# Optimization experiments

Measured on AMD Instinct MI355X. Metric: run time of the kernel, lower is better.

The kernel has to match this reference:

```python
import jax, jax.numpy as jnp
import numpy as np

B, S, E, H = 4, 2048, 1024, 16
D = E // H  # head_dim = 64

def setup_inputs() -> dict:
    key = jax.random.key(0)
    k1, k2, k3 = jax.random.split(key, 3)
    x = jax.random.normal(k1, (B, S, E), dtype=jnp.float32)
    # Linear weights stored as [in, out] so y = x @ W (torch Linear uses W^T; same math).
    w_att = jax.random.normal(k2, (E, 3 * E), dtype=jnp.float32) * (1.0 / np.sqrt(E))
    w_proj = jax.random.normal(k3, (E, E), dtype=jnp.float32) * (1.0 / np.sqrt(E))
    return {"x": x, "w_att": w_att, "w_proj": w_proj}

def reference(x, w_att, w_proj):
    b, s, e = x.shape
    qkv = x @ w_att                      # [b, s, 3e]
    q, k, v = jnp.split(qkv, 3, axis=-1)
    # [b, h, s, d]
    q = q.reshape(b, s, H, D).transpose(0, 2, 1, 3)
    k = k.reshape(b, s, H, D).transpose(0, 2, 1, 3)
    v = v.reshape(b, s, H, D).transpose(0, 2, 1, 3)
    scale = 1.0 / np.sqrt(D)
    att = jnp.einsum('bhqd,bhkd->bhqk', q, k) * scale  # [b, h, s, s]
    causal = jnp.tril(jnp.ones((s, s), dtype=bool))
    att = jnp.where(causal[None, None], att, jnp.finfo(att.dtype).min)
    att = jax.nn.softmax(att, axis=-1)
    y = jnp.einsum('bhqk,bhkd->bhqd', att, v)          # [b, h, s, d]
    y = y.transpose(0, 2, 1, 3).reshape(b, s, e)
    return y @ w_proj
```

## Files before the change

kernel.cpp:

```cpp
#include <hip/hip_runtime.h>
#include <hip/hip_bf16.h>

typedef __bf16 b16v8 __attribute__((ext_vector_type(8)));
typedef __bf16 b16v4 __attribute__((ext_vector_type(4)));
typedef float  f32x4 __attribute__((ext_vector_type(4)));

#define BB 4
#define SS 2048
#define EE 1024
#define HH 16
#define DD 64

#define QSCALE 0.18033688011112042f
#define CMAX 20.0f

__device__ __forceinline__ void async16(const __bf16* g, __bf16* l) {
  typedef __attribute__((address_space(1))) const unsigned int gu32;
  typedef __attribute__((address_space(3))) unsigned int lu32;
  __builtin_amdgcn_global_load_lds((gu32*)g, (lu32*)l, 16, 0, 0);
}

__device__ __forceinline__ f32x4 mfma16x16x16_bf16(b16v4 a, b16v4 b, f32x4 c) {
#if __has_builtin(__builtin_amdgcn_mfma_f32_16x16x16_bf16)
  return __builtin_amdgcn_mfma_f32_16x16x16_bf16(a, b, c, 0, 0, 0);
#else
  typedef short s16v4 __attribute__((ext_vector_type(4)));
  union U { b16v4 h; s16v4 s; };
  U ua, ub; ua.h = a; ub.h = b;
  return __builtin_amdgcn_mfma_f32_16x16x16bf16_1k(ua.s, ub.s, c, 0, 0, 0);
#endif
}

__global__ __launch_bounds__(256) void cast_x_kernel(const float* __restrict__ in,
                                                     __bf16* __restrict__ out, int n4) {
  int i = blockIdx.x * 256 + threadIdx.x;
  if (i >= n4) return;
  float4 f = ((const float4*)in)[i];
  b16v4 o = {(__bf16)f.x, (__bf16)f.y, (__bf16)f.z, (__bf16)f.w};
  ((b16v4*)out)[i] = o;
}

__global__ __launch_bounds__(256) void cast_transpose(const float* __restrict__ w,
                                                      __bf16* __restrict__ wt, int K, int N) {
  __shared__ float t[32][33];
  int n0 = blockIdx.x * 32, k0 = blockIdx.y * 32;
  int tx = threadIdx.x & 31, ty = threadIdx.x >> 5;
#pragma unroll
  for (int j = 0; j < 32; j += 8)
    t[ty + j][tx] = w[(size_t)(k0 + ty + j) * N + n0 + tx];
  __syncthreads();
#pragma unroll
  for (int j = 0; j < 32; j += 8)
    wt[(size_t)(n0 + ty + j) * K + k0 + tx] = (__bf16)t[tx][ty + j];
}

template <int EPI>
__global__ __launch_bounds__(256) void gemm_bt(const __bf16* __restrict__ A,
                                               const __bf16* __restrict__ Bt,
                                               void* C0, void* C1, void* C2,
                                               int M, int N, int K) {
  __shared__ __bf16 a_lds[2][128 * 32];
  __shared__ __bf16 b_lds[2][128 * 32];
  const int tid = threadIdx.x;
  const int lane = tid & 63;
  const int w = tid >> 6;
  const int wm = (w >> 1) * 64, wn = (w & 1) * 64;
  const int l16 = lane & 15, quad = lane >> 4;
  const __bf16* Ab = A + (size_t)blockIdx.y * 128 * K;
  const __bf16* Bb = Bt + (size_t)blockIdx.x * 128 * K;

  auto stage = [&](int k0, int bufi) {
#pragma unroll
    for (int i = 0; i < 2; ++i) {
      int c = tid + i * 256;
      int row = c >> 2, ch = c & 3;
      async16(Ab + (size_t)row * K + k0 + ((ch ^ (row & 3)) * 8), a_lds[bufi] + c * 8);
    }
#pragma unroll
    for (int i = 0; i < 2; ++i) {
      int c = tid + i * 256;
      int row = c >> 2, ch = c & 3;
      async16(Bb + (size_t)row * K + k0 + ((ch ^ (row & 3)) * 8), b_lds[bufi] + c * 8);
    }
  };

  f32x4 acc[4][4];
#pragma unroll
  for (int i = 0; i < 4; ++i)
#pragma unroll
    for (int j = 0; j < 4; ++j) acc[i][j] = f32x4{0.f, 0.f, 0.f, 0.f};

  stage(0, 0);
  const int KT = K >> 5;
  const int sw = (quad ^ (l16 & 3)) * 8;
  for (int kt = 0; kt < KT; ++kt) {
    __syncthreads();
    if (kt + 1 < KT) stage((kt + 1) << 5, (kt + 1) & 1);
    const __bf16* ab = a_lds[kt & 1];
    const __bf16* bb = b_lds[kt & 1];
    b16v8 af[4], bf4[4];
#pragma unroll
    for (int t = 0; t < 4; ++t) {
      af[t] = *(const b16v8*)(ab + (wm + t * 16 + l16) * 32 + sw);
      bf4[t] = *(const b16v8*)(bb + (wn + t * 16 + l16) * 32 + sw);
    }
#pragma unroll
    for (int mt = 0; mt < 4; ++mt)
#pragma unroll
      for (int nt = 0; nt < 4; ++nt)
        acc[mt][nt] = __builtin_amdgcn_mfma_f32_16x16x32_bf16(af[mt], bf4[nt], acc[mt][nt], 0, 0, 0);
  }

  if (EPI == 0) {
    __bf16* qb = (__bf16*)C0;
    __bf16* kb = (__bf16*)C1;
    __bf16* vtb = (__bf16*)C2;
#pragma unroll
    for (int mt = 0; mt < 4; ++mt)
#pragma unroll
      for (int nt = 0; nt < 4; ++nt) {
        int row = blockIdx.y * 128 + wm + mt * 16 + quad * 4;
        int col = blockIdx.x * 128 + wn + nt * 16 + l16;
        int b = row >> 11, s = row & 2047;
        int sec = col >> 10, cc = col & 1023;
        int h = cc >> 6, d = cc & 63;
        if (sec == 2) {
          b16v4 vv = {(__bf16)acc[mt][nt][0], (__bf16)acc[mt][nt][1],
                      (__bf16)acc[mt][nt][2], (__bf16)acc[mt][nt][3]};
          *(b16v4*)(vtb + ((size_t)(b * HH + h) * DD + d) * SS + s) = vv;
        } else {
          __bf16* dst = (sec == 0) ? qb : kb;
          float sc = (sec == 0) ? QSCALE : 1.0f;
#pragma unroll
          for (int r = 0; r < 4; ++r)
            dst[(((size_t)(b * HH + h) * SS + s + r) << 6) + d] = (__bf16)(acc[mt][nt][r] * sc);
        }
      }
  } else {
    float* out = (float*)C0;
#pragma unroll
    for (int mt = 0; mt < 4; ++mt)
#pragma unroll
      for (int nt = 0; nt < 4; ++nt)
#pragma unroll
        for (int r = 0; r < 4; ++r) {
          int row = blockIdx.y * 128 + wm + mt * 16 + quad * 4 + r;
          int col = blockIdx.x * 128 + wn + nt * 16 + l16;
          out[(size_t)row * N + col] = acc[mt][nt][r];
        }
  }
}

__global__ __launch_bounds__(256, 4) void attn_kernel(const __bf16* __restrict__ qb,
                                                      const __bf16* __restrict__ kb,
                                                      const __bf16* __restrict__ vtb,
                                                      __bf16* __restrict__ y) {
  __shared__ __bf16 kv_lds[2][8192];
  const int tid = threadIdx.x;
  const int lane = tid & 63;
  const int w = tid >> 6;
  const int l16 = lane & 15, quad = lane >> 4;
  const int bh = blockIdx.x, p = blockIdx.y;
  const int b = bh >> 4, h = bh & 15;
  const __bf16* kbase = kb + (size_t)bh * SS * DD;
  const __bf16* vtbase = vtb + (size_t)bh * DD * SS;

  const int e = l16 & 7;
  const int koff0 = l16 * 64 + ((quad ^ e) * 8);
  const int koff1 = l16 * 64 + (((quad + 4) ^ e) * 8);
  int voff[4];
#pragma unroll
  for (int kf = 0; kf < 4; ++kf)
    voff[kf] = 4096 + l16 * 64 + (((kf * 2 + (quad >> 1)) ^ e) * 8) + ((quad & 1) * 4);

  int gK[2], gV[2], lK[2], lV[2];
#pragma unroll
  for (int i = 0; i < 2; ++i) {
    int L = tid + i * 256;
    int row = L >> 3, c = L & 7;
    gK[i] = row * DD + ((c ^ (row & 7)) * 8);
    lK[i] = L * 8;
    gV[i] = row * SS + ((c ^ (row & 7)) * 8);
    lV[i] = 4096 + L * 8;
  }
  auto stage = [&](int j, __bf16* buf) {
    const __bf16* kj = kbase + j * (64 * DD);
    const __bf16* vj = vtbase + j * 64;
#pragma unroll
    for (int i = 0; i < 2; ++i) async16(kj + gK[i], buf + lK[i]);
#pragma unroll
    for (int i = 0; i < 2; ++i) async16(vj + gV[i], buf + lV[i]);
  };

#pragma unroll
  for (int t = 0; t < 2; ++t) {
    const int qt = (t == 0) ? (31 - p) : p;

    b16v8 qf[2];
#pragma unroll
    for (int ks = 0; ks < 2; ++ks)
      qf[ks] = *(const b16v8*)(qb + ((size_t)bh * SS + qt * 64 + w * 16 + l16) * DD + ks * 32 + quad * 8);

    f32x4 o[4];
#pragma unroll
    for (int dt = 0; dt < 4; ++dt) o[dt] = f32x4{0.f, 0.f, 0.f, 0.f};
    f32x4 lv = {0.f, 0.f, 0.f, 0.f};

    __syncthreads();
    stage(0, kv_lds[0]);

    for (int j = 0; j <= qt; ++j) {
      __syncthreads();
      if (j < qt) stage(j + 1, kv_lds[(j + 1) & 1]);
      const __bf16* buf = kv_lds[0] + ((j & 1) << 13);

      f32x4 s[4];
#pragma unroll
      for (int kf = 0; kf < 4; ++kf) s[kf] = f32x4{-CMAX, -CMAX, -CMAX, -CMAX};
#pragma unroll
      for (int kf = 0; kf < 4; ++kf) {
        b16v8 k0 = *(const b16v8*)(buf + koff0 + kf * 1024);
        b16v8 k1 = *(const b16v8*)(buf + koff1 + kf * 1024);
        s[kf] = __builtin_amdgcn_mfma_f32_16x16x32_bf16(k0, qf[0], s[kf], 0, 0, 0);
        s[kf] = __builtin_amdgcn_mfma_f32_16x16x32_bf16(k1, qf[1], s[kf], 0, 0, 0);
      }
      if (j == qt) {
        int ql = w * 16 + l16;
#pragma unroll
        for (int kf = 0; kf < 4; ++kf)
#pragma unroll
          for (int r = 0; r < 4; ++r)
            if (kf * 16 + quad * 4 + r > ql) s[kf][r] = -1e30f;
      }
#pragma unroll
      for (int kf = 0; kf < 4; ++kf)
#pragma unroll
        for (int r = 0; r < 4; ++r) s[kf][r] = __builtin_amdgcn_exp2f(s[kf][r]);
      lv += (s[0] + s[1]) + (s[2] + s[3]);
#pragma unroll
      for (int kf = 0; kf < 4; ++kf) {
        b16v4 pf = {(__bf16)s[kf][0], (__bf16)s[kf][1], (__bf16)s[kf][2], (__bf16)s[kf][3]};
#pragma unroll
        for (int dt = 0; dt < 4; ++dt) {
          b16v4 vf = *(const b16v4*)(buf + voff[kf] + dt * 1024);
          o[dt] = mfma16x16x16_bf16(vf, pf, o[dt]);
        }
      }
    }

    float lr = (lv[0] + lv[1]) + (lv[2] + lv[3]);
    lr += __shfl_xor(lr, 16);
    lr += __shfl_xor(lr, 32);
    float inv = 1.0f / lr;
    int q = qt * 64 + w * 16 + l16;
#pragma unroll
    for (int dt = 0; dt < 4; ++dt) {
      b16v4 ov = {(__bf16)(o[dt][0] * inv), (__bf16)(o[dt][1] * inv),
                  (__bf16)(o[dt][2] * inv), (__bf16)(o[dt][3] * inv)};
      *(b16v4*)(y + ((size_t)b * SS + q) * EE + h * 64 + dt * 16 + quad * 4) = ov;
    }
  }
}

extern "C" void kernel_launch(void* const* d_in, const int* in_sizes, int n_in,
                              void* d_out, int out_size, void* d_ws, size_t ws_size,
                              hipStream_t stream) {
  (void)in_sizes; (void)n_in; (void)out_size; (void)ws_size;
  const float* x = (const float*)d_in[0];
  const float* w_att = (const float*)d_in[1];
  const float* w_proj = (const float*)d_in[2];
  float* out = (float*)d_out;

  char* ws = (char*)d_ws;
  size_t off = 0;
  auto alloc = [&](size_t elems) { __bf16* p = (__bf16*)(ws + off); off += elems * 2; return p; };
  __bf16* xb = alloc(8388608);
  __bf16* qb = alloc(8388608);
  __bf16* kb = alloc(8388608);
  __bf16* vtb = alloc(8388608);
  __bf16* watt = alloc(3145728);
  __bf16* wproj = alloc(1048576);

  cast_x_kernel<<<8192, 256, 0, stream>>>(x, xb, 2097152);
  cast_transpose<<<dim3(96, 32), 256, 0, stream>>>(w_att, watt, 1024, 3072);
  cast_transpose<<<dim3(32, 32), 256, 0, stream>>>(w_proj, wproj, 1024, 1024);
  gemm_bt<0><<<dim3(24, 64), 256, 0, stream>>>(xb, watt, qb, kb, vtb, 8192, 3072, 1024);
  attn_kernel<<<dim3(64, 16), 256, 0, stream>>>(qb, kb, vtb, xb);
  gemm_bt<1><<<dim3(8, 64), 256, 0, stream>>>(xb, wproj, out, nullptr, nullptr, 8192, 1024, 1024);
}
```

Baseline: 246.2 us.

## Replace GEMM with 256x256-tile 8-wave kernel with XCD-aware block remap

Replaces the 128x128 bf16 GEMM with a 256x256 tile, 512-thread kernel that uses 64-wide K steps and an 8-chunk XOR-swizzled LDS layout. The A and B stage loads are interleaved with four MFMA quadrants, separated by barriers and s_setprio to overlap global-to-LDS copies with compute. Block ids are remapped so that neighbouring tiles land on the same XCD, which is meant to improve L2 reuse. The larger tile raises arithmetic intensity and cuts redundant global loads, at the cost of much higher register and LDS use and a small grid (128 blocks for the projection GEMM).

```diff
diff --git a/kernel.cpp b/kernel.cpp
--- a/kernel.cpp
+++ b/kernel.cpp
@@ -55,60 +55,147 @@
 }
 
 template <int EPI>
-__global__ __launch_bounds__(256) void gemm_bt(const __bf16* __restrict__ A,
-                                               const __bf16* __restrict__ Bt,
-                                               void* C0, void* C1, void* C2,
-                                               int M, int N, int K) {
-  __shared__ __bf16 a_lds[2][128 * 32];
-  __shared__ __bf16 b_lds[2][128 * 32];
+__global__ __launch_bounds__(512, 2) void gemm256(const __bf16* __restrict__ A,
+                                                  const __bf16* __restrict__ Bt,
+                                                  void* C0, void* C1, void* C2,
+                                                  int M, int N, int K) {
+  __shared__ __bf16 lds[2][32768];
   const int tid = threadIdx.x;
   const int lane = tid & 63;
-  const int w = tid >> 6;
-  const int wm = (w >> 1) * 64, wn = (w & 1) * 64;
+  const int wid = tid >> 6;
+  const int wm = (wid >> 2) * 128;
+  const int wn = (wid & 3) * 64;
   const int l16 = lane & 15, quad = lane >> 4;
-  const __bf16* Ab = A + (size_t)blockIdx.y * 128 * K;
-  const __bf16* Bb = Bt + (size_t)blockIdx.x * 128 * K;
-
-  auto stage = [&](int k0, int bufi) {
+
+  const int gx = gridDim.x, gy = gridDim.y;
+  const int nwg = gx * gy;
+  const int bid = blockIdx.y * gx + blockIdx.x;
+  const int qq = nwg >> 3, rr = nwg & 7;
+  const int xcd = bid & 7, idx = bid >> 3;
+  const int wgid = (xcd < rr ? xcd * (qq + 1) : rr * (qq + 1) + (xcd - rr) * qq) + idx;
+  const int bx = wgid % gx, by = wgid / gx;
+
+  const __bf16* Ab = A + (size_t)by * 256 * K;
+  const __bf16* Bb = Bt + (size_t)bx * 256 * K;
+
+  const __bf16 *sA[4], *sB[4];
+  int ldst[4];
+#pragma unroll
+  for (int h = 0; h < 2; ++h)
 #pragma unroll
     for (int i = 0; i < 2; ++i) {
-      int c = tid + i * 256;
-      int row = c >> 2, ch = c & 3;
-      async16(Ab + (size_t)row * K + k0 + ((ch ^ (row & 3)) * 8), a_lds[bufi] + c * 8);
-    }
-#pragma unroll
-    for (int i = 0; i < 2; ++i) {
-      int c = tid + i * 256;
-      int row = c >> 2, ch = c & 3;
-      async16(Bb + (size_t)row * K + k0 + ((ch ^ (row & 3)) * 8), b_lds[bufi] + c * 8);
-    }
+      int L = tid + i * 512;
+      int row = L >> 3, c = L & 7;
+      int sw = (c ^ (row & 7)) * 8;
+      sA[h * 2 + i] = Ab + (size_t)(h * 128 + row) * K + sw;
+      sB[h * 2 + i] = Bb + (size_t)(h * 128 + row) * K + sw;
+      ldst[h * 2 + i] = h * 8192 + L * 8;
+    }
+  auto stageA = [&](int bi, int t) {
+#pragma unroll
+    for (int j = 0; j < 4; ++j) async16(sA[j] + (t << 6), &lds[bi][ldst[j]]);
   };
-
-  f32x4 acc[4][4];
-#pragma unroll
-  for (int i = 0; i < 4; ++i)
+  auto stageB = [&](int bi, int t) {
+#pragma unroll
+    for (int j = 0; j < 4; ++j) async16(sB[j] + (t << 6), &lds[bi][16384 + ldst[j]]);
+  };
+
+  const int aB = (wm + l16) * 64;
+  const int bB = 16384 + (wn + l16) * 64;
+  const int e7 = l16 & 7;
+  const int swz0 = (quad ^ e7) * 8;
+  const int swz1 = ((4 + quad) ^ e7) * 8;
+
+  f32x4 acc[8][4];
+#pragma unroll
+  for (int i = 0; i < 8; ++i)
 #pragma unroll
     for (int j = 0; j < 4; ++j) acc[i][j] = f32x4{0.f, 0.f, 0.f, 0.f};
 
-  stage(0, 0);
-  const int KT = K >> 5;
-  const int sw = (quad ^ (l16 & 3)) * 8;
+  stageA(0, 0);
+  stageB(0, 0);
+  asm volatile("s_waitcnt vmcnt(0)" ::: "memory");
+  __builtin_amdgcn_s_barrier();
+
+  const int KT = K >> 6;
   for (int kt = 0; kt < KT; ++kt) {
-    __syncthreads();
-    if (kt + 1 < KT) stage((kt + 1) << 5, (kt + 1) & 1);
-    const __bf16* ab = a_lds[kt & 1];
-    const __bf16* bb = b_lds[kt & 1];
-    b16v8 af[4], bf4[4];
-#pragma unroll
-    for (int t = 0; t < 4; ++t) {
-      af[t] = *(const b16v8*)(ab + (wm + t * 16 + l16) * 32 + sw);
-      bf4[t] = *(const b16v8*)(bb + (wn + t * 16 + l16) * 32 + sw);
-    }
+    const __bf16* bufp = lds[kt & 1];
+    const int nb = (kt + 1) & 1;
+    const bool more = (kt + 1) < KT;
+    b16v8 a[4][2], b0[2][2], b1[2][2];
+
+#pragma unroll
+    for (int mt = 0; mt < 4; ++mt) {
+      a[mt][0] = *(const b16v8*)(bufp + aB + mt * 1024 + swz0);
+      a[mt][1] = *(const b16v8*)(bufp + aB + mt * 1024 + swz1);
+    }
+#pragma unroll
+    for (int nt = 0; nt < 2; ++nt) {
+      b0[nt][0] = *(const b16v8*)(bufp + bB + nt * 1024 + swz0);
+      b0[nt][1] = *(const b16v8*)(bufp + bB + nt * 1024 + swz1);
+    }
+    if (more) stageA(nb, kt + 1);
+    __builtin_amdgcn_s_barrier();
+    asm volatile("s_waitcnt lgkmcnt(0)" ::: "memory");
+    __builtin_amdgcn_s_setprio(1);
 #pragma unroll
     for (int mt = 0; mt < 4; ++mt)
 #pragma unroll
-      for (int nt = 0; nt < 4; ++nt)
-        acc[mt][nt] = __builtin_amdgcn_mfma_f32_16x16x32_bf16(af[mt], bf4[nt], acc[mt][nt], 0, 0, 0);
+      for (int nt = 0; nt < 2; ++nt)
+#pragma unroll
+        for (int ks = 0; ks < 2; ++ks)
+          acc[mt][nt] = __builtin_amdgcn_mfma_f32_16x16x32_bf16(a[mt][ks], b0[nt][ks], acc[mt][nt], 0, 0, 0);
+    __builtin_amdgcn_s_setprio(0);
+    __builtin_amdgcn_s_barrier();
+
+#pragma unroll
+    for (int nt = 0; nt < 2; ++nt) {
+      b1[nt][0] = *(const b16v8*)(bufp + bB + (2 + nt) * 1024 + swz0);
+      b1[nt][1] = *(const b16v8*)(bufp + bB + (2 + nt) * 1024 + swz1);
+    }
+    if (more) stageB(nb, kt + 1);
+    __builtin_amdgcn_s_barrier();
+    asm volatile("s_waitcnt lgkmcnt(0)" ::: "memory");
+    __builtin_amdgcn_s_setprio(1);
+#pragma unroll
+    for (int mt = 0; mt < 4; ++mt)
+#pragma unroll
+      for (int nt = 0; nt < 2; ++nt)
+#pragma unroll
+        for (int ks = 0; ks < 2; ++ks)
+          acc[mt][2 + nt] = __builtin_amdgcn_mfma_f32_16x16x32_bf16(a[mt][ks], b1[nt][ks], acc[mt][2 + nt], 0, 0, 0);
+    __builtin_amdgcn_s_setprio(0);
+    __builtin_amdgcn_s_barrier();
+
+#pragma unroll
+    for (int mt = 0; mt < 4; ++mt) {
+      a[mt][0] = *(const b16v8*)(bufp + aB + 4096 + mt * 1024 + swz0);
+      a[mt][1] = *(const b16v8*)(bufp + aB + 4096 + mt * 1024 + swz1);
+    }
+    __builtin_amdgcn_s_barrier();
+    asm volatile("s_waitcnt lgkmcnt(0)" ::: "memory");
+    __builtin_amdgcn_s_setprio(1);
+#pragma unroll
+    for (int mt = 0; mt < 4; ++mt)
+#pragma unroll
+      for (int nt = 0; nt < 2; ++nt)
+#pragma unroll
+        for (int ks = 0; ks < 2; ++ks)
+          acc[4 + mt][2 + nt] = __builtin_amdgcn_mfma_f32_16x16x32_bf16(a[mt][ks], b1[nt][ks], acc[4 + mt][2 + nt], 0, 0, 0);
+    __builtin_amdgcn_s_setprio(0);
+    __builtin_amdgcn_s_barrier();
+
+    __builtin_amdgcn_s_setprio(1);
+#pragma unroll
+    for (int mt = 0; mt < 4; ++mt)
+#pragma unroll
+      for (int nt = 0; nt < 2; ++nt)
+#pragma unroll
+        for (int ks = 0; ks < 2; ++ks)
+          acc[4 + mt][nt] = __builtin_amdgcn_mfma_f32_16x16x32_bf16(a[mt][ks], b0[nt][ks], acc[4 + mt][nt], 0, 0, 0);
+    __builtin_amdgcn_s_setprio(0);
+    asm volatile("s_waitcnt vmcnt(0)" ::: "memory");
+    __builtin_amdgcn_s_barrier();
   }
 
   if (EPI == 0) {
@@ -116,11 +203,11 @@
     __bf16* kb = (__bf16*)C1;
     __bf16* vtb = (__bf16*)C2;
 #pragma unroll
-    for (int mt = 0; mt < 4; ++mt)
+    for (int mt = 0; mt < 8; ++mt)
 #pragma unroll
       for (int nt = 0; nt < 4; ++nt) {
-        int row = blockIdx.y * 128 + wm + mt * 16 + quad * 4;
-        int col = blockIdx.x * 128 + wn + nt * 16 + l16;
+        int row = by * 256 + wm + mt * 16 + quad * 4;
+        int col = bx * 256 + wn + nt * 16 + l16;
         int b = row >> 11, s = row & 2047;
         int sec = col >> 10, cc = col & 1023;
         int h = cc >> 6, d = cc & 63;
@@ -139,15 +226,15 @@
   } else {
     float* out = (float*)C0;
 #pragma unroll
-    for (int mt = 0; mt < 4; ++mt)
-#pragma unroll
-      for (int nt = 0; nt < 4; ++nt)
-#pragma unroll
-        for (int r = 0; r < 4; ++r) {
-          int row = blockIdx.y * 128 + wm + mt * 16 + quad * 4 + r;
-          int col = blockIdx.x * 128 + wn + nt * 16 + l16;
-          out[(size_t)row * N + col] = acc[mt][nt][r];
-        }
+    for (int mt = 0; mt < 8; ++mt)
+#pragma unroll
+      for (int nt = 0; nt < 4; ++nt) {
+        int row = by * 256 + wm + mt * 16 + quad * 4;
+        int col = bx * 256 + wn + nt * 16 + l16;
+#pragma unroll
+        for (int r = 0; r < 4; ++r)
+          out[(size_t)(row + r) * N + col] = acc[mt][nt][r];
+      }
   }
 }
 
@@ -284,7 +371,7 @@
   cast_x_kernel<<<8192, 256, 0, stream>>>(x, xb, 2097152);
   cast_transpose<<<dim3(96, 32), 256, 0, stream>>>(w_att, watt, 1024, 3072);
   cast_transpose<<<dim3(32, 32), 256, 0, stream>>>(w_proj, wproj, 1024, 1024);
-  gemm_bt<0><<<dim3(24, 64), 256, 0, stream>>>(xb, watt, qb, kb, vtb, 8192, 3072, 1024);
+  gemm256<0><<<dim3(12, 32), 512, 0, stream>>>(xb, watt, qb, kb, vtb, 8192, 3072, 1024);
   attn_kernel<<<dim3(64, 16), 256, 0, stream>>>(qb, kb, vtb, xb);
-  gemm_bt<1><<<dim3(8, 64), 256, 0, stream>>>(xb, wproj, out, nullptr, nullptr, 8192, 1024, 1024);
-}
+  gemm256<1><<<dim3(4, 32), 512, 0, stream>>>(xb, wproj, out, nullptr, nullptr, 8192, 1024, 1024);
+}
```

Result: no change. 250.7 us (+1.8%).
